# Kernel optimization log

Hardware: AMD Instinct MI355X
Metric: run time of the kernel (lower is better)

## Reference

```python
import jax, jax.numpy as jnp
import numpy as np

B = 1
H_IMG, W_IMG = 64, 64
NF = H_IMG * W_IMG          # 4096 front/query tokens
NS = 1024                   # satellite tokens (32x32 grid)
SAT_IN, FRONT_IN = 768, 320
NH, HD = 8, 64
MD = NH * HD                # 512
GHID, GHD = 128, 16
GMD = NH * GHD              # 128
GEO_RATIO, ROPE_BASE = 0.5, 10000.0
LAMBDA_GEO, LAMBDA_GEOM = 1.0, 1.0
EPS = 1e-5


def _linear(x, w, b):
    return x @ w.T + b


def _layernorm(x, g, b):
    m = x.mean(-1, keepdims=True)
    v = jnp.var(x, axis=-1, keepdims=True)
    return (x - m) / jnp.sqrt(v + EPS) * g + b


def _georope(t, xy):
    """Continuous 2D (x,y) rotary embedding on the first GEO_RATIO fraction of head_dim.
    t: [B,NH,N,HD], xy: [B,N,2]."""
    rot = int(HD * GEO_RATIO)       # rotated dims (32)
    axis = rot // 2                 # dims per spatial axis (16)
    half = axis // 2                # frequency pairs per axis (8)
    inv_freq = ROPE_BASE ** (-jnp.arange(half, dtype=t.dtype) / half)

    def rot_axis(a, coord):
        th = coord[:, None, :, None] * inv_freq   # [B,1,N,half]
        c, s = jnp.cos(th), jnp.sin(th)
        a1, a2 = a[..., :half], a[..., half:]
        return jnp.concatenate([a1 * c - a2 * s, a1 * s + a2 * c], axis=-1)

    tx = rot_axis(t[..., :axis], xy[..., 0])
    ty = rot_axis(t[..., axis:rot], xy[..., 1])
    return jnp.concatenate([tx, ty, t[..., rot:]], axis=-1)


def _heads(x, hd):
    b, n, _ = x.shape
    return x.reshape(b, n, NH, hd).transpose(0, 2, 1, 3)


def setup_inputs() -> dict:
    key = jax.random.key(0)
    ks = iter(jax.random.split(key, 64))

    def w(*shape):
        return jax.random.normal(next(ks), shape, jnp.float32) / np.sqrt(shape[-1]).astype(np.float32)

    z = lambda n: jnp.zeros((n,), jnp.float32)
    o = lambda n: jnp.ones((n,), jnp.float32)
    return {
        "front_feat": jax.random.normal(next(ks), (B, FRONT_IN, H_IMG, W_IMG), jnp.float32),
        "front_bev_xy": jax.random.uniform(next(ks), (B, NF, 2), jnp.float32, -1.0, 1.0),
        "sat_tokens": jax.random.normal(next(ks), (B, NS, SAT_IN), jnp.float32),
        "sat_xy": jax.random.uniform(next(ks), (B, NS, 2), jnp.float32, -1.0, 1.0),
        "front_plucker": jax.random.normal(next(ks), (B, NF, 6), jnp.float32),
        "pos_w1": w(MD, 2), "pos_b1": z(MD), "pos_w2": w(MD, MD), "pos_b2": z(MD),
        "fa_w": w(MD, FRONT_IN), "fa_b": z(MD), "fa_ln_g": o(MD), "fa_ln_b": z(MD),
        "qn_g": o(MD), "qn_b": z(MD),
        "sa_w": w(MD, SAT_IN), "sa_b": z(MD), "sa_ln_g": o(MD), "sa_ln_b": z(MD),
        "wq": w(MD, MD), "bq": z(MD), "wk": w(MD, MD), "bk": z(MD), "wv": w(MD, MD), "bv": z(MD),
        "plk_w1": w(GHID, 6), "plk_b1": z(GHID), "plk_w2": w(GHID, GHID), "plk_b2": z(GHID),
        "sxy_w1": w(GHID, 2), "sxy_b1": z(GHID), "sxy_w2": w(GHID, GHID), "sxy_b2": z(GHID),
        "gqn_g": o(GHID), "gqn_b": z(GHID), "gkn_g": o(GHID), "gkn_b": z(GHID),
        "wqg": w(GMD, GHID), "bqg": z(GMD), "wkg": w(GMD, GHID), "bkg": z(GMD),
    }


def reference(front_feat, front_bev_xy, sat_tokens, sat_xy, front_plucker,
              pos_w1, pos_b1, pos_w2, pos_b2, fa_w, fa_b, fa_ln_g, fa_ln_b,
              qn_g, qn_b, sa_w, sa_b, sa_ln_g, sa_ln_b, wq, bq, wk, bk, wv, bv,
              plk_w1, plk_b1, plk_w2, plk_b2, sxy_w1, sxy_b1, sxy_w2, sxy_b2,
              gqn_g, gqn_b, gkn_g, gkn_b, wqg, bqg, wkg, bkg):
    b = front_feat.shape[0]
    ff = front_feat.reshape(b, FRONT_IN, NF).transpose(0, 2, 1)      # [B,NF,C]
    pos = _linear(jax.nn.silu(_linear(front_bev_xy, pos_w1, pos_b1)), pos_w2, pos_b2)
    feat = _layernorm(_linear(ff, fa_w, fa_b), fa_ln_g, fa_ln_b)
    q_embed = _layernorm(pos + feat, qn_g, qn_b)
    sat_feat = _layernorm(_linear(sat_tokens, sa_w, sa_b), sa_ln_g, sa_ln_b)
    q = _heads(_linear(q_embed, wq, bq), HD)                         # [B,H,NF,HD]
    k = _heads(_linear(sat_feat, wk, bk), HD)                        # [B,H,NS,HD]
    v = _heads(_linear(sat_feat, wv, bv), HD)
    qr = _georope(q, front_bev_xy)
    kr = _georope(k, sat_xy)
    logits = jnp.einsum('bhqd,bhkd->bhqk', qr, kr) / np.float32(np.sqrt(HD))
    # learned geometric Q/K stream (Plucker rays vs sat xy)
    plk = _layernorm(_linear(jax.nn.silu(_linear(front_plucker, plk_w1, plk_b1)), plk_w2, plk_b2), gqn_g, gqn_b)
    sgf = _layernorm(_linear(jax.nn.silu(_linear(sat_xy, sxy_w1, sxy_b1)), sxy_w2, sxy_b2), gkn_g, gkn_b)
    qg = _heads(_linear(plk, wqg, bqg), GHD)
    kg = _heads(_linear(sgf, wkg, bkg), GHD)
    logits = logits + LAMBDA_GEOM * (jnp.einsum('bhqd,bhkd->bhqk', qg, kg) / np.float32(np.sqrt(GHD)))
    # additive pairwise squared-distance bias, broadcast over heads
    dist2 = ((front_bev_xy[:, :, None, :] - sat_xy[:, None, :, :]) ** 2).sum(-1)   # [B,NF,NS]
    logits = logits - LAMBDA_GEO * dist2[:, None]
    attn = jax.nn.softmax(logits, axis=-1)
    read = jnp.einsum('bhqk,bhkd->bhqd', attn, v)
    return read.transpose(0, 2, 1, 3).reshape(b, NF, MD)
```

## Files before the change

### kernel.cpp

```cpp
#include <hip/hip_runtime.h>
#include <hip/hip_bf16.h>
#include <stdint.h>

#define NF 4096
#define NS 1024
#define MD 512
#define HD 64
#define DA 96
#define GHID 128

#define L2E 1.44269504f
#define S2L 1.6986436f
#define SMAX 12.0f
#define NSPLIT 2

typedef unsigned short u16;
typedef __attribute__((ext_vector_type(8))) short bf8v;
typedef __attribute__((ext_vector_type(4))) float f4v;

__device__ __forceinline__ u16 f2bf(float f) {
  __hip_bfloat16 h = __float2bfloat16(f);
  return __builtin_bit_cast(u16, h);
}
__device__ __forceinline__ float bf2f(u16 u) {
  union { unsigned u; float f; } v; v.u = ((unsigned)u) << 16; return v.f;
}
__device__ __forceinline__ f4v mfma16(bf8v a, bf8v b, f4v c) {
  return __builtin_amdgcn_mfma_f32_16x16x32_bf16(a, b, c, 0, 0, 0);
}
__device__ __forceinline__ void gld16(const void* g, void* l) {
  __builtin_amdgcn_global_load_lds(
      (const __attribute__((address_space(1))) unsigned int*)g,
      (__attribute__((address_space(3))) unsigned int*)l, 16, 0, 0);
}

__device__ __forceinline__ size_t kfidx(int h, int n, int d) {
  return ((((size_t)(h * 16 + (n >> 6)) * 4 + ((n >> 4) & 3)) * 3 + (d >> 5)) * 64
          + ((d >> 3) & 3) * 16 + (n & 15)) * 8 + (d & 7);
}
__device__ __forceinline__ size_t vfidx(int h, int n, int dv) {
  return ((((size_t)(h * 16 + (n >> 6)) * 2 + ((n >> 5) & 1)) * 4 + (dv >> 4)) * 64
          + ((n >> 3) & 3) * 16 + (dv & 15)) * 8 + (n & 7);
}

#define OFF_POSW2 0
#define OFF_FAW   262144
#define OFF_SAW   425984
#define OFF_WQ    819200
#define OFF_WKV   1081344
#define OFF_PLKW2 1605632
#define OFF_SXYW2 1622016
#define OFF_WQG   1638400
#define OFF_WKG   1654784
#define OFF_SATT  1671168
#define TOTW      2457600

#define EPI_OUT   0
#define EPI_ROPE  1
#define EPI_VT    2
#define EPI_GEO   3
#define EPI_ROPEK 4
#define EPI_GEOK  5

__global__ __launch_bounds__(256) void k_l0(
    const float* __restrict__ s0, const float* __restrict__ s1,
    const float* __restrict__ s2, const float* __restrict__ s3,
    const float* __restrict__ s4, const float* __restrict__ s5,
    const float* __restrict__ s6, const float* __restrict__ s7,
    const float* __restrict__ s8, const float* __restrict__ s9,
    const float* __restrict__ s10, u16* __restrict__ pool,
    const float* __restrict__ bk, const float* __restrict__ bv,
    float* __restrict__ bkv,
    const float* __restrict__ ff, u16* __restrict__ ffT,
    const float* __restrict__ in0, const float* __restrict__ w0,
    const float* __restrict__ b0, u16* __restrict__ o0,
    const float* __restrict__ in1, const float* __restrict__ w1,
    const float* __restrict__ b1, u16* __restrict__ o1,
    const float* __restrict__ in2, const float* __restrict__ w2,
    const float* __restrict__ b2, u16* __restrict__ o2,
    u16* __restrict__ Qaug, u16* __restrict__ Kf, float* __restrict__ kk2) {
  __shared__ u16 sT[32][72];
  int blk = blockIdx.x, t = threadIdx.x;
  if (blk < 2401) {
    int i4 = blk * 256 + t;
    if (i4 < TOTW / 4) {
      int idx = i4 * 4;
      const float* src; int off;
      if      (idx < OFF_FAW)   { src = s0;  off = OFF_POSW2; }
      else if (idx < OFF_SAW)   { src = s1;  off = OFF_FAW; }
      else if (idx < OFF_WQ)    { src = s2;  off = OFF_SAW; }
      else if (idx < OFF_WKV)   { src = s3;  off = OFF_WQ; }
      else if (idx < 1343488)   { src = s4;  off = OFF_WKV; }
      else if (idx < OFF_PLKW2) { src = s5;  off = 1343488; }
      else if (idx < OFF_SXYW2) { src = s6;  off = OFF_PLKW2; }
      else if (idx < OFF_WQG)   { src = s7;  off = OFF_SXYW2; }
      else if (idx < OFF_WKG)   { src = s8;  off = OFF_WQG; }
      else if (idx < OFF_SATT)  { src = s9;  off = OFF_WKG; }
      else                      { src = s10; off = OFF_SATT; }
      float4 v = *(const float4*)(src + (idx - off));
      ushort4 o;
      o.x = f2bf(v.x); o.y = f2bf(v.y); o.z = f2bf(v.z); o.w = f2bf(v.w);
      *(ushort4*)(pool + idx) = o;
    } else if (i4 < TOTW / 4 + 256) {
      int j = (i4 - TOTW / 4) * 4;
#pragma unroll
      for (int e = 0; e < 4; ++e) {
        int b = j + e;
        bkv[b] = (b < 512) ? bk[b] : bv[b - 512];
      }
    }
  } else if (blk < 3041) {
    int lb = blk - 2401;
    int n0 = (lb & 63) * 64, c0 = (lb >> 6) * 32;
    {
      int cr = t >> 3, nc = (t & 7) * 8;
      const float* src = ff + (size_t)(c0 + cr) * NF + n0 + nc;
      float4 v0 = *(const float4*)src, v1 = *(const float4*)(src + 4);
      bf8v p;
      p[0]=(short)f2bf(v0.x); p[1]=(short)f2bf(v0.y); p[2]=(short)f2bf(v0.z); p[3]=(short)f2bf(v0.w);
      p[4]=(short)f2bf(v1.x); p[5]=(short)f2bf(v1.y); p[6]=(short)f2bf(v1.z); p[7]=(short)f2bf(v1.w);
      *(bf8v*)&sT[cr][nc] = p;
    }
    __syncthreads();
    {
      int r = t >> 2, cc = (t & 3) * 8;
      bf8v p;
#pragma unroll
      for (int e = 0; e < 8; ++e) p[e] = (short)sT[cc + e][r];
      *(bf8v*)(ffT + (size_t)(n0 + r) * 320 + c0 + cc) = p;
    }
  } else if (blk < 13793) {
    int lb = blk - 3041;
    const float *in, *w, *b; u16* o; int mlog, K, idx;
    if (lb < 8192)       { in = in0; w = w0; b = b0; o = o0; mlog = 9; K = 2; idx = lb * 256 + t; }
    else if (lb < 10240) { in = in1; w = w1; b = b1; o = o1; mlog = 7; K = 6; idx = (lb - 8192) * 256 + t; }
    else                 { in = in2; w = w2; b = b2; o = o2; mlog = 7; K = 2; idx = (lb - 10240) * 256 + t; }
    int M = 1 << mlog;
    int n = idx >> mlog, m = idx & (M - 1);
    float acc = b[m];
    for (int k = 0; k < K; ++k) acc += in[n * K + k] * w[m * K + k];
    o[idx] = f2bf(acc / (1.f + __expf(-acc)));
  } else {
    int id = (blk - 13793) * 256 + t;
    int side = id >= NF * 8;
    int lid = side ? id - NF * 8 : id;
    int n = lid >> 3, h = lid & 7;
    const float* xy = side ? in2 : in0;
    float x = xy[n * 2], y = xy[n * 2 + 1];
    bf8v p0, z;
#pragma unroll
    for (int e = 0; e < 8; ++e) { p0[e] = 0; z[e] = 0; }
    p0[0] = (short)f2bf(S2L * x);
    p0[1] = (short)f2bf(S2L * y);
    if (!side) {
      u16* dst = Qaug + ((size_t)h * NF + n) * DA + 80;
      *(bf8v*)dst = p0;
      *(bf8v*)(dst + 8) = z;
    } else {
      int t8 = n >> 6, jj = (n >> 4) & 3, l16 = n & 15;
      size_t base = (((size_t)(h * 16 + t8) * 4 + jj) * 3 + 2) * 64;
      *(bf8v*)(Kf + (base + 32 + l16) * 8) = p0;
      *(bf8v*)(Kf + (base + 48 + l16) * 8) = z;
      if (h == 0) kk2[n] = L2E * (x * x + y * y) + SMAX;
    }
  }
}

__device__ __forceinline__ void gemm_body128(const u16* __restrict__ A, const u16* __restrict__ W,
                                             const float* __restrict__ bias, u16* __restrict__ out,
                                             int m0, int n0, int N, int K) {
  __shared__ u16 sA[2][128 * 64];
  __shared__ u16 sB[2][64 * 64];
  const int tid = threadIdx.x, w = tid >> 6, lane = tid & 63;
  const int l16 = lane & 15, lh = lane >> 4;

  f4v acc[2][4];
#pragma unroll
  for (int m = 0; m < 2; ++m)
#pragma unroll
    for (int j = 0; j < 4; ++j) acc[m][j] = (f4v){0.f, 0.f, 0.f, 0.f};

  auto stageA = [&](int buf, int k0) {
#pragma unroll
    for (int i = 0; i < 4; ++i) {
      int c = i * 256 + tid;
      int row = c >> 3, cp = c & 7;
      int sc_ = cp ^ (row & 7);
      gld16(A + (size_t)(m0 + row) * K + k0 + sc_ * 8, &sA[buf][c * 8]);
    }
  };
  auto stageB = [&](int buf, int k0) {
#pragma unroll
    for (int i = 0; i < 2; ++i) {
      int c = i * 256 + tid;
      int row = c >> 3, cp = c & 7;
      int sc_ = cp ^ (row & 7);
      gld16(W + (size_t)(n0 + row) * K + k0 + sc_ * 8, &sB[buf][c * 8]);
    }
  };

  stageA(0, 0); stageB(0, 0);
  __syncthreads();
  const int NK = K >> 6;
  for (int ks = 0; ks < NK; ++ks) {
    int nb = ks & 1;
    if (ks + 1 < NK) { stageA(nb ^ 1, (ks + 1) * 64); stageB(nb ^ 1, (ks + 1) * 64); }
#pragma unroll
    for (int kk = 0; kk < 2; ++kk) {
      bf8v af[2], bfr[4];
#pragma unroll
      for (int m = 0; m < 2; ++m) {
        int row = w * 32 + m * 16 + l16;
        int cp = (kk * 4 + lh) ^ (row & 7);
        af[m] = *(const bf8v*)&sA[nb][row * 64 + cp * 8];
      }
#pragma unroll
      for (int j = 0; j < 4; ++j) {
        int row = j * 16 + l16;
        int cp = (kk * 4 + lh) ^ (row & 7);
        bfr[j] = *(const bf8v*)&sB[nb][row * 64 + cp * 8];
      }
#pragma unroll
      for (int m = 0; m < 2; ++m)
#pragma unroll
        for (int j = 0; j < 4; ++j) acc[m][j] = mfma16(af[m], bfr[j], acc[m][j]);
    }
    __syncthreads();
  }
#pragma unroll
  for (int m = 0; m < 2; ++m) {
    int grow = m0 + w * 32 + m * 16 + (lh << 2);
#pragma unroll
    for (int j = 0; j < 4; ++j) {
      int gcol = n0 + j * 16 + l16;
      float bvs = bias ? bias[gcol] : 0.f;
#pragma unroll
      for (int r = 0; r < 4; ++r)
        out[(size_t)(grow + r) * N + gcol] = f2bf(acc[m][j][r] + bvs);
    }
  }
}

__device__ __forceinline__ void gemm_body(const u16* __restrict__ A, const u16* __restrict__ W,
                                          const float* __restrict__ bias, u16* __restrict__ out,
                                          int m0, int n0, int N, int K,
                                          int mode, float scale, const float* __restrict__ xy,
                                          u16* __restrict__ aug, int nrows) {
  constexpr int MR = 2, NR = 2;
  __shared__ u16 sA[2][64 * 64];
  __shared__ u16 sB[2][64 * 64];
  const int tid = threadIdx.x, w = tid >> 6, lane = tid & 63;
  const int l16 = lane & 15, lh = lane >> 4;
  const int wr = w >> 1, wc = w & 1;

  f4v acc[MR][NR];
#pragma unroll
  for (int m = 0; m < MR; ++m)
#pragma unroll
    for (int j = 0; j < NR; ++j) acc[m][j] = (f4v){0.f, 0.f, 0.f, 0.f};

  auto stageA = [&](int buf, int k0) {
#pragma unroll
    for (int i = 0; i < 2; ++i) {
      int c = i * 256 + tid;
      int row = c >> 3, cp = c & 7;
      int sc_ = cp ^ (row & 7);
      gld16(A + (size_t)(m0 + row) * K + k0 + sc_ * 8, &sA[buf][c * 8]);
    }
  };
  auto stageB = [&](int buf, int k0) {
#pragma unroll
    for (int i = 0; i < 2; ++i) {
      int c = i * 256 + tid;
      int row = c >> 3, cp = c & 7;
      int sc_ = cp ^ (row & 7);
      gld16(W + (size_t)(n0 + row) * K + k0 + sc_ * 8, &sB[buf][c * 8]);
    }
  };

  stageA(0, 0); stageB(0, 0);
  __syncthreads();
  const int NK = K >> 6;
  for (int ks = 0; ks < NK; ++ks) {
    int nb = ks & 1;
    if (ks + 1 < NK) { stageA(nb ^ 1, (ks + 1) * 64); stageB(nb ^ 1, (ks + 1) * 64); }
#pragma unroll
    for (int kk = 0; kk < 2; ++kk) {
      bf8v af[MR], bfr[NR];
#pragma unroll
      for (int m = 0; m < MR; ++m) {
        int row = wr * 32 + m * 16 + l16;
        int cp = (kk * 4 + lh) ^ (row & 7);
        af[m] = *(const bf8v*)&sA[nb][row * 64 + cp * 8];
      }
#pragma unroll
      for (int j = 0; j < NR; ++j) {
        int row = wc * 32 + j * 16 + l16;
        int cp = (kk * 4 + lh) ^ (row & 7);
        bfr[j] = *(const bf8v*)&sB[nb][row * 64 + cp * 8];
      }
#pragma unroll
      for (int m = 0; m < MR; ++m)
#pragma unroll
        for (int j = 0; j < NR; ++j) acc[m][j] = mfma16(af[m], bfr[j], acc[m][j]);
    }
    __syncthreads();
  }

  if (mode == EPI_OUT) {
#pragma unroll
    for (int m = 0; m < MR; ++m) {
      int grow = m0 + wr * 32 + m * 16 + (lh << 2);
#pragma unroll
      for (int j = 0; j < NR; ++j) {
        int gcol = n0 + wc * 32 + j * 16 + l16;
        float bvs = bias ? bias[gcol] : 0.f;
#pragma unroll
        for (int r = 0; r < 4; ++r)
          out[(size_t)(grow + r) * N + gcol] = f2bf(acc[m][j][r] + bvs);
      }
    }
  } else if (mode == EPI_ROPE || mode == EPI_ROPEK) {
    float fr = __expf(-(float)(l16 & 7) * 1.1512925465f);
#pragma unroll
    for (int m = 0; m < MR; ++m) {
      int grow = m0 + wr * 32 + m * 16 + (lh << 2);
#pragma unroll
      for (int j = 0; j < NR; ++j) {
        int gcol = n0 + wc * 32 + j * 16 + l16;
        int h = gcol >> 6, d = gcol & 63;
        float bvs = bias[gcol];
#pragma unroll
        for (int r = 0; r < 4; ++r) {
          int n = grow + r;
          float val = acc[m][j][r] + bvs;
          float part = __shfl_xor(val, 8);
          float outv = val;
          if (wc == 0) {
            float2 c2 = ((const float2*)xy)[n];
            float coord = j ? c2.y : c2.x;
            float sn, cs;
            __sincosf(coord * fr, &sn, &cs);
            outv = (l16 & 8) ? (part * sn + val * cs) : (val * cs - part * sn);
          }
          if (mode == EPI_ROPE)
            aug[((size_t)h * nrows + n) * DA + d] = f2bf(outv * scale);
          else
            aug[kfidx(h, n, d)] = f2bf(outv * scale);
        }
      }
    }
  } else if (mode == EPI_VT) {
#pragma unroll
    for (int m = 0; m < MR; ++m) {
      int grow = m0 + wr * 32 + m * 16 + (lh << 2);
#pragma unroll
      for (int j = 0; j < NR; ++j) {
        int gcol = n0 + wc * 32 + j * 16 + l16;
        int vcol = gcol - 512;
        int h = vcol >> 6, dv = vcol & 63;
        float bvs = bias[gcol];
        ushort4 o;
        o.x = f2bf(acc[m][j][0] + bvs);
        o.y = f2bf(acc[m][j][1] + bvs);
        o.z = f2bf(acc[m][j][2] + bvs);
        o.w = f2bf(acc[m][j][3] + bvs);
        *(ushort4*)(aug + vfidx(h, grow, dv)) = o;
      }
    }
  } else {
#pragma unroll
    for (int m = 0; m < MR; ++m) {
      int grow = m0 + wr * 32 + m * 16 + (lh << 2);
#pragma unroll
      for (int j = 0; j < NR; ++j) {
        int gcol = n0 + wc * 32 + j * 16 + l16;
        int h = gcol >> 4, dg = gcol & 15;
        float bvs = bias[gcol];
#pragma unroll
        for (int r = 0; r < 4; ++r) {
          float ov = (acc[m][j][r] + bvs) * scale;
          if (mode == EPI_GEO)
            aug[((size_t)h * nrows + grow + r) * DA + 64 + dg] = f2bf(ov);
          else
            aug[kfidx(h, grow + r, 64 + dg)] = f2bf(ov);
        }
      }
    }
  }
}

struct GP { const u16* A; const u16* W; const float* bias; u16* out;
            int K; int N; int M; int mode; float scale; const float* xy;
            u16* aug; int nrows; };

__device__ __forceinline__ void gemm_dispatch128(const GP& g, int blk) {
  int mt = g.M >> 7;
  int m0 = (blk % mt) * 128, n0 = (blk / mt) * 64;
  gemm_body128(g.A, g.W, g.bias, g.out, m0, n0, g.N, g.K);
}
__device__ __forceinline__ void gemm_dispatch(const GP& g, int blk) {
  int mt = g.M >> 6;
  int m0 = (blk % mt) * 64, n0 = (blk / mt) * 64;
  gemm_body(g.A, g.W, g.bias, g.out, m0, n0, g.N, g.K,
            g.mode, g.scale, g.xy, g.aug, g.nrows);
}

__global__ __launch_bounds__(256) void k_gemm_L1(GP a, GP b, GP c, GP d, GP e) {
  int blk = blockIdx.x;
  if (blk < 256)       gemm_dispatch128(a, blk);
  else if (blk < 512)  gemm_dispatch128(b, blk - 256);
  else if (blk < 576)  gemm_dispatch128(c, blk - 512);
  else if (blk < 640)  gemm_dispatch128(d, blk - 576);
  else                 gemm_dispatch128(e, blk - 640);
}
__global__ __launch_bounds__(256) void k_gemm_L2(GP a, GP b, GP c, GP d, u16* Vfp) {
  int blk = blockIdx.x;
  if (blk < 512) {
    gemm_dispatch(a, blk);
  } else if (blk < 768) {
    int lb = blk - 512;
    int m0 = (lb & 15) * 64, n0 = (lb >> 4) * 64;
    if (n0 >= 512)
      gemm_body(b.A, b.W, b.bias, b.out, m0, n0, b.N, b.K, EPI_VT, 1.f, nullptr, Vfp, NS);
    else
      gemm_body(b.A, b.W, b.bias, b.out, m0, n0, b.N, b.K, b.mode, b.scale, b.xy, b.aug, b.nrows);
  } else if (blk < 896) {
    gemm_dispatch(c, blk - 768);
  } else {
    gemm_dispatch(d, blk - 896);
  }
}

__global__ __launch_bounds__(256) void k_ln_all(
    const u16* __restrict__ feat_pre, const u16* __restrict__ pos,
    const float* __restrict__ fg, const float* __restrict__ fb,
    const float* __restrict__ qg, const float* __restrict__ qb2,
    u16* __restrict__ q_embed,
    const u16* __restrict__ satf_pre, const float* __restrict__ sg,
    const float* __restrict__ sb, u16* __restrict__ satf,
    const u16* __restrict__ ginq, const u16* __restrict__ gink,
    const float* __restrict__ ggq, const float* __restrict__ gbq,
    const float* __restrict__ ggk, const float* __restrict__ gbk,
    u16* __restrict__ goutq, u16* __restrict__ goutk) {
  int blk = blockIdx.x;
  int w = threadIdx.x >> 6, lane = threadIdx.x & 63;
  if (blk < 1024) {
    int row = blk * 4 + w;
    bf8v v = *(const bf8v*)(feat_pre + (size_t)row * 512 + lane * 8);
    float x[8];
#pragma unroll
    for (int e = 0; e < 8; ++e) x[e] = bf2f((u16)v[e]);
    float s = 0.f, q = 0.f;
#pragma unroll
    for (int e = 0; e < 8; ++e) { s += x[e]; q += x[e] * x[e]; }
#pragma unroll
    for (int mm = 1; mm < 64; mm <<= 1) { s += __shfl_xor(s, mm); q += __shfl_xor(q, mm); }
    float mean = s / 512.f, var = q / 512.f - mean * mean;
    float rstd = rsqrtf(var + 1e-5f);
    bf8v vp = *(const bf8v*)(pos + (size_t)row * 512 + lane * 8);
#pragma unroll
    for (int e = 0; e < 8; ++e)
      x[e] = (x[e] - mean) * rstd * fg[lane * 8 + e] + fb[lane * 8 + e] + bf2f((u16)vp[e]);
    s = 0.f; q = 0.f;
#pragma unroll
    for (int e = 0; e < 8; ++e) { s += x[e]; q += x[e] * x[e]; }
#pragma unroll
    for (int mm = 1; mm < 64; mm <<= 1) { s += __shfl_xor(s, mm); q += __shfl_xor(q, mm); }
    mean = s / 512.f; var = q / 512.f - mean * mean;
    rstd = rsqrtf(var + 1e-5f);
    bf8v ov;
#pragma unroll
    for (int e = 0; e < 8; ++e)
      ov[e] = (short)f2bf((x[e] - mean) * rstd * qg[lane * 8 + e] + qb2[lane * 8 + e]);
    *(bf8v*)(q_embed + (size_t)row * 512 + lane * 8) = ov;
  } else if (blk < 1280) {
    int row = (blk - 1024) * 4 + w;
    bf8v v = *(const bf8v*)(satf_pre + (size_t)row * 512 + lane * 8);
    float x[8];
#pragma unroll
    for (int e = 0; e < 8; ++e) x[e] = bf2f((u16)v[e]);
    float s = 0.f, q = 0.f;
#pragma unroll
    for (int e = 0; e < 8; ++e) { s += x[e]; q += x[e] * x[e]; }
#pragma unroll
    for (int mm = 1; mm < 64; mm <<= 1) { s += __shfl_xor(s, mm); q += __shfl_xor(q, mm); }
    float mean = s / 512.f, var = q / 512.f - mean * mean;
    float rstd = rsqrtf(var + 1e-5f);
    bf8v ov;
#pragma unroll
    for (int e = 0; e < 8; ++e)
      ov[e] = (short)f2bf((x[e] - mean) * rstd * sg[lane * 8 + e] + sb[lane * 8 + e]);
    *(bf8v*)(satf + (size_t)row * 512 + lane * 8) = ov;
  } else {
    int row = (blk - 1280) * 4 + w;
    const u16* in; const float *g, *b; u16* out;
    if (row < 4096) { in = ginq; g = ggq; b = gbq; out = goutq; }
    else { row -= 4096; in = gink; g = ggk; b = gbk; out = goutk; }
    uint32_t v = *(const uint32_t*)(in + (size_t)row * 128 + lane * 2);
    float x0 = bf2f((u16)(v & 0xffff)), x1 = bf2f((u16)(v >> 16));
    float s = x0 + x1, q = x0 * x0 + x1 * x1;
#pragma unroll
    for (int mm = 1; mm < 64; mm <<= 1) { s += __shfl_xor(s, mm); q += __shfl_xor(q, mm); }
    float mean = s / 128.f, var = q / 128.f - mean * mean;
    float rstd = rsqrtf(var + 1e-5f);
    u16 o0 = f2bf((x0 - mean) * rstd * g[lane * 2] + b[lane * 2]);
    u16 o1 = f2bf((x1 - mean) * rstd * g[lane * 2 + 1] + b[lane * 2 + 1]);
    *(uint32_t*)(out + (size_t)row * 128 + lane * 2) = (uint32_t)o0 | ((uint32_t)o1 << 16);
  }
}

__global__ __launch_bounds__(256, 4) void k_flash(const u16* __restrict__ Qa,
                                                  const u16* __restrict__ Kf,
                                                  const u16* __restrict__ Vf,
                                                  const float* __restrict__ kk2,
                                                  u16* __restrict__ Opart,
                                                  float* __restrict__ lbuf) {
  const int h = blockIdx.y, qb = blockIdx.x, sp = blockIdx.z;
  const int tid = threadIdx.x, w = tid >> 6, lane = tid & 63;
  const int l16 = lane & 15, lh = lane >> 4;
  __shared__ u16 sP[4][16][68];
  __shared__ float sKK[512];

  ((float2*)sKK)[tid] = ((const float2*)(kk2 + sp * 512))[tid];

  const int qrow = qb * 64 + w * 16 + l16;
  bf8v qf[3];
#pragma unroll
  for (int c = 0; c < 3; ++c)
    qf[c] = *(const bf8v*)(Qa + (size_t)(h * NF + qrow) * DA + c * 32 + lh * 8);

  bf8v ONES;
#pragma unroll
  for (int i = 0; i < 8; ++i) ONES[i] = (short)0x3F80;

  const int crow = qb * 64 + w * 16 + (lh << 2);
  float l_run[4] = {0.f, 0.f, 0.f, 0.f};
  f4v accO[4];
#pragma unroll
  for (int d = 0; d < 4; ++d) accO[d] = (f4v){0.f, 0.f, 0.f, 0.f};

  const int kt0 = sp * (NS / 64 / NSPLIT);
  __syncthreads();

  const int NT = NS / 64 / NSPLIT;
  for (int t8 = 0; t8 < NT; ++t8) {
    const int T = kt0 + t8;
    const u16* kfb = Kf + (size_t)(h * 16 + T) * 4 * 3 * 64 * 8;
    const u16* vfb = Vf + (size_t)(h * 16 + T) * 2 * 4 * 64 * 8;
#pragma unroll
    for (int j = 0; j < 4; ++j) {
      f4v s4 = (f4v){0.f, 0.f, 0.f, 0.f};
#pragma unroll
      for (int c = 0; c < 3; ++c) {
        bf8v kf = *(const bf8v*)(kfb + (size_t)((j * 3 + c) * 64 + lane) * 8);
        s4 = mfma16(qf[c], kf, s4);
      }
      float ck = sKK[t8 * 64 + j * 16 + l16];
#pragma unroll
      for (int r = 0; r < 4; ++r) {
        float pv = exp2f(s4[r] - ck);
        sP[w][(lh << 2) + r][j * 16 + l16] = f2bf(pv);
      }
    }
    bf8v pf0 = *(const bf8v*)&sP[w][l16][lh * 8];
    bf8v pf1 = *(const bf8v*)&sP[w][l16][32 + lh * 8];
    f4v ls = (f4v){0.f, 0.f, 0.f, 0.f};
    ls = mfma16(pf0, ONES, ls);
    ls = mfma16(pf1, ONES, ls);
#pragma unroll
    for (int r = 0; r < 4; ++r) l_run[r] += ls[r];
#pragma unroll
    for (int c = 0; c < 2; ++c) {
      bf8v pf = (c == 0) ? pf0 : pf1;
#pragma unroll
      for (int d = 0; d < 4; ++d) {
        bf8v vf = *(const bf8v*)(vfb + (size_t)((c * 4 + d) * 64 + lane) * 8);
        accO[d] = mfma16(pf, vf, accO[d]);
      }
    }
  }
  size_t obase = (size_t)(sp * 8 + h) * NF + crow;
#pragma unroll
  for (int d = 0; d < 4; ++d)
#pragma unroll
    for (int r = 0; r < 4; ++r)
      Opart[(obase + r) * 64 + d * 16 + l16] = f2bf(accO[d][r]);
  if (l16 == 0) {
#pragma unroll
    for (int r = 0; r < 4; ++r) lbuf[obase + r] = l_run[r];
  }
}

__global__ void k_combine(const u16* __restrict__ Opart, const float* __restrict__ lbuf,
                          float* __restrict__ out) {
  int i4 = blockIdx.x * 256 + threadIdx.x;
  int n = i4 >> 7;
  int c4 = i4 & 127, h = c4 >> 4, d4 = c4 & 15;
  float l = 0.f, ox = 0.f, oy = 0.f, oz = 0.f, ow = 0.f;
#pragma unroll
  for (int s2 = 0; s2 < NSPLIT; ++s2) {
    size_t base = (size_t)(s2 * 8 + h) * NF + n;
    l += lbuf[base];
    ushort4 a = ((const ushort4*)(Opart + base * 64))[d4];
    ox += bf2f(a.x); oy += bf2f(a.y); oz += bf2f(a.z); ow += bf2f(a.w);
  }
  float rl = 1.f / l;
  ((float4*)out)[i4] = make_float4(ox * rl, oy * rl, oz * rl, ow * rl);
}

extern "C" void kernel_launch(void* const* d_in, const int* in_sizes, int n_in,
                              void* d_out, int out_size, void* d_ws, size_t ws_size,
                              hipStream_t stream) {
  (void)in_sizes; (void)n_in; (void)out_size; (void)ws_size;
  const float* front_feat = (const float*)d_in[0];
  const float* bev_xy     = (const float*)d_in[1];
  const float* sat_tokens = (const float*)d_in[2];
  const float* sat_xy     = (const float*)d_in[3];
  const float* plucker    = (const float*)d_in[4];
  const float* pos_w1 = (const float*)d_in[5];
  const float* pos_b1 = (const float*)d_in[6];
  const float* pos_w2 = (const float*)d_in[7];
  const float* pos_b2 = (const float*)d_in[8];
  const float* fa_w   = (const float*)d_in[9];
  const float* fa_b   = (const float*)d_in[10];
  const float* fa_ln_g = (const float*)d_in[11];
  const float* fa_ln_b = (const float*)d_in[12];
  const float* qn_g   = (const float*)d_in[13];
  const float* qn_b   = (const float*)d_in[14];
  const float* sa_w   = (const float*)d_in[15];
  const float* sa_b   = (const float*)d_in[16];
  const float* sa_ln_g = (const float*)d_in[17];
  const float* sa_ln_b = (const float*)d_in[18];
  const float* wq = (const float*)d_in[19];
  const float* bq = (const float*)d_in[20];
  const float* wk = (const float*)d_in[21];
  const float* bk = (const float*)d_in[22];
  const float* wv = (const float*)d_in[23];
  const float* bv = (const float*)d_in[24];
  const float* plk_w1 = (const float*)d_in[25];
  const float* plk_b1 = (const float*)d_in[26];
  const float* plk_w2 = (const float*)d_in[27];
  const float* plk_b2 = (const float*)d_in[28];
  const float* sxy_w1 = (const float*)d_in[29];
  const float* sxy_b1 = (const float*)d_in[30];
  const float* sxy_w2 = (const float*)d_in[31];
  const float* sxy_b2 = (const float*)d_in[32];
  const float* gqn_g = (const float*)d_in[33];
  const float* gqn_b = (const float*)d_in[34];
  const float* gkn_g = (const float*)d_in[35];
  const float* gkn_b = (const float*)d_in[36];
  const float* wqg = (const float*)d_in[37];
  const float* bqg = (const float*)d_in[38];
  const float* wkg = (const float*)d_in[39];
  const float* bkg = (const float*)d_in[40];

  char* ws = (char*)d_ws;
  size_t off = 0;
  auto alloc = [&](size_t bytes) {
    size_t r = off;
    off += (bytes + 255) & ~(size_t)255;
    return r;
  };
  u16*   wpool   = (u16*)(ws + alloc((size_t)TOTW * 2));
  float* bkv     = (float*)(ws + alloc(1024 * 4));
  u16*   ffT     = (u16*)(ws + alloc((size_t)NF * 320 * 2));
  u16*   pos_h   = (u16*)(ws + alloc((size_t)NF * MD * 2));
  u16*   plk_h   = (u16*)(ws + alloc((size_t)NF * GHID * 2));
  u16*   sxy_h   = (u16*)(ws + alloc((size_t)NS * GHID * 2));
  u16*   pos     = (u16*)(ws + alloc((size_t)NF * MD * 2));
  u16*   feat_pre= (u16*)(ws + alloc((size_t)NF * MD * 2));
  u16*   satf_pre= (u16*)(ws + alloc((size_t)NS * MD * 2));
  u16*   satf    = (u16*)(ws + alloc((size_t)NS * MD * 2));
  u16*   q_embed = (u16*)(ws + alloc((size_t)NF * MD * 2));
  u16*   plk2    = (u16*)(ws + alloc((size_t)NF * GHID * 2));
  u16*   sxy2    = (u16*)(ws + alloc((size_t)NS * GHID * 2));
  u16*   Qaug    = (u16*)(ws + alloc((size_t)8 * NF * DA * 2));
  u16*   Kf      = (u16*)(ws + alloc((size_t)8 * NS * DA * 2));
  u16*   Vf      = (u16*)(ws + alloc((size_t)8 * HD * NS * 2));
  float* kk2     = (float*)(ws + alloc((size_t)NS * 4));
  u16*   Opart   = (u16*)(ws + alloc((size_t)NSPLIT * 8 * NF * 64 * 2));
  float* lbuf    = (float*)(ws + alloc((size_t)NSPLIT * 8 * NF * 4));
  u16* plk_ln = plk_h;
  u16* sgf    = sxy_h;

  dim3 b256(256);
  k_l0<<<dim3(13953), b256, 0, stream>>>(
      pos_w2, fa_w, sa_w, wq, wk, wv, plk_w2, sxy_w2, wqg, wkg, sat_tokens,
      wpool, bk, bv, bkv, front_feat, ffT,
      bev_xy, pos_w1, pos_b1, pos_h,
      plucker, plk_w1, plk_b1, plk_h,
      sat_xy, sxy_w1, sxy_b1, sxy_h,
      Qaug, Kf, kk2);

  GP gpos {pos_h, wpool + OFF_POSW2, pos_b2, pos, 512, 512, 4096, EPI_OUT, 0.f, nullptr, nullptr, 0};
  GP gfeat{ffT, wpool + OFF_FAW, fa_b, feat_pre, 320, 512, 4096, EPI_OUT, 0.f, nullptr, nullptr, 0};
  GP gsat {wpool + OFF_SATT, wpool + OFF_SAW, sa_b, satf_pre, 768, 512, 1024, EPI_OUT, 0.f, nullptr, nullptr, 0};
  GP ggq1 {plk_h, wpool + OFF_PLKW2, plk_b2, plk2, 128, 128, 4096, EPI_OUT, 0.f, nullptr, nullptr, 0};
  GP ggk1 {sxy_h, wpool + OFF_SXYW2, sxy_b2, sxy2, 128, 128, 1024, EPI_OUT, 0.f, nullptr, nullptr, 0};
  k_gemm_L1<<<dim3(656), b256, 0, stream>>>(gpos, gfeat, gsat, ggq1, ggk1);

  k_ln_all<<<dim3(2560), b256, 0, stream>>>(
      feat_pre, pos, fa_ln_g, fa_ln_b, qn_g, qn_b, q_embed,
      satf_pre, sa_ln_g, sa_ln_b, satf,
      plk2, sxy2, gqn_g, gqn_b, gkn_g, gkn_b, plk_ln, sgf);

  GP gq  {q_embed, wpool + OFF_WQ, bq, nullptr, 512, 512, 4096, EPI_ROPE, 0.125f * L2E, bev_xy, Qaug, NF};
  GP gkv {satf, wpool + OFF_WKV, bkv, nullptr, 512, 1024, 1024, EPI_ROPEK, 1.f, sat_xy, Kf, NS};
  GP ggq2{plk_ln, wpool + OFF_WQG, bqg, nullptr, 128, 128, 4096, EPI_GEO, 0.25f * L2E, nullptr, Qaug, NF};
  GP ggk2{sgf, wpool + OFF_WKG, bkg, nullptr, 128, 128, 1024, EPI_GEOK, 1.f, nullptr, Kf, NS};
  k_gemm_L2<<<dim3(928), b256, 0, stream>>>(gq, gkv, ggq2, ggk2, Vf);

  k_flash<<<dim3(NF / 64, 8, NSPLIT), b256, 0, stream>>>(Qaug, Kf, Vf, kk2, Opart, lbuf);
  k_combine<<<dim3(NF * MD / 4 / 256), b256, 0, stream>>>(Opart, lbuf, (float*)d_out);
}
```

Measured before the change: 79.74 us.

## Merge split-K flash halves within one block and drop combine kernel

```diff
diff --git a/kernel.cpp b/kernel.cpp
--- a/kernel.cpp
+++ b/kernel.cpp
@@ -12,7 +12,6 @@
 #define L2E 1.44269504f
 #define S2L 1.6986436f
 #define SMAX 12.0f
-#define NSPLIT 2
 
 typedef unsigned short u16;
 typedef __attribute__((ext_vector_type(8))) short bf8v;
@@ -510,19 +509,22 @@
   }
 }
 
-__global__ __launch_bounds__(256, 4) void k_flash(const u16* __restrict__ Qa,
+__global__ __launch_bounds__(512, 2) void k_flash(const u16* __restrict__ Qa,
                                                   const u16* __restrict__ Kf,
                                                   const u16* __restrict__ Vf,
                                                   const float* __restrict__ kk2,
-                                                  u16* __restrict__ Opart,
-                                                  float* __restrict__ lbuf) {
-  const int h = blockIdx.y, qb = blockIdx.x, sp = blockIdx.z;
-  const int tid = threadIdx.x, w = tid >> 6, lane = tid & 63;
+                                                  float* __restrict__ out) {
+  const int h = blockIdx.y, qb = blockIdx.x;
+  const int tid = threadIdx.x;
+  const int half = tid >> 8, t = tid & 255;
+  const int w = t >> 6, lane = t & 63;
   const int l16 = lane & 15, lh = lane >> 4;
-  __shared__ u16 sP[4][16][68];
-  __shared__ float sKK[512];
-
-  ((float2*)sKK)[tid] = ((const float2*)(kk2 + sp * 512))[tid];
+  __shared__ u16 sP[8][16][68];
+  __shared__ float sKK[1024];
+  __shared__ float xO[256 * 16];
+  __shared__ float xl[256 * 4];
+
+  ((float2*)sKK)[tid] = ((const float2*)kk2)[tid];
 
   const int qrow = qb * 64 + w * 16 + l16;
   bf8v qf[3];
@@ -540,12 +542,10 @@
 #pragma unroll
   for (int d = 0; d < 4; ++d) accO[d] = (f4v){0.f, 0.f, 0.f, 0.f};
 
-  const int kt0 = sp * (NS / 64 / NSPLIT);
   __syncthreads();
 
-  const int NT = NS / 64 / NSPLIT;
-  for (int t8 = 0; t8 < NT; ++t8) {
-    const int T = kt0 + t8;
+  for (int t8 = 0; t8 < 8; ++t8) {
+    const int T = half * 8 + t8;
     const u16* kfb = Kf + (size_t)(h * 16 + T) * 4 * 3 * 64 * 8;
     const u16* vfb = Vf + (size_t)(h * 16 + T) * 2 * 4 * 64 * 8;
 #pragma unroll
@@ -556,15 +556,15 @@
         bf8v kf = *(const bf8v*)(kfb + (size_t)((j * 3 + c) * 64 + lane) * 8);
         s4 = mfma16(qf[c], kf, s4);
       }
-      float ck = sKK[t8 * 64 + j * 16 + l16];
+      float ck = sKK[T * 64 + j * 16 + l16];
 #pragma unroll
       for (int r = 0; r < 4; ++r) {
         float pv = exp2f(s4[r] - ck);
-        sP[w][(lh << 2) + r][j * 16 + l16] = f2bf(pv);
-      }
-    }
-    bf8v pf0 = *(const bf8v*)&sP[w][l16][lh * 8];
-    bf8v pf1 = *(const bf8v*)&sP[w][l16][32 + lh * 8];
+        sP[half * 4 + w][(lh << 2) + r][j * 16 + l16] = f2bf(pv);
+      }
+    }
+    bf8v pf0 = *(const bf8v*)&sP[half * 4 + w][l16][lh * 8];
+    bf8v pf1 = *(const bf8v*)&sP[half * 4 + w][l16][32 + lh * 8];
     f4v ls = (f4v){0.f, 0.f, 0.f, 0.f};
     ls = mfma16(pf0, ONES, ls);
     ls = mfma16(pf1, ONES, ls);
@@ -580,33 +580,28 @@
       }
     }
   }
-  size_t obase = (size_t)(sp * 8 + h) * NF + crow;
-#pragma unroll
-  for (int d = 0; d < 4; ++d)
-#pragma unroll
-    for (int r = 0; r < 4; ++r)
-      Opart[(obase + r) * 64 + d * 16 + l16] = f2bf(accO[d][r]);
-  if (l16 == 0) {
-#pragma unroll
-    for (int r = 0; r < 4; ++r) lbuf[obase + r] = l_run[r];
-  }
-}
-
-__global__ void k_combine(const u16* __restrict__ Opart, const float* __restrict__ lbuf,
-                          float* __restrict__ out) {
-  int i4 = blockIdx.x * 256 + threadIdx.x;
-  int n = i4 >> 7;
-  int c4 = i4 & 127, h = c4 >> 4, d4 = c4 & 15;
-  float l = 0.f, ox = 0.f, oy = 0.f, oz = 0.f, ow = 0.f;
-#pragma unroll
-  for (int s2 = 0; s2 < NSPLIT; ++s2) {
-    size_t base = (size_t)(s2 * 8 + h) * NF + n;
-    l += lbuf[base];
-    ushort4 a = ((const ushort4*)(Opart + base * 64))[d4];
-    ox += bf2f(a.x); oy += bf2f(a.y); oz += bf2f(a.z); ow += bf2f(a.w);
-  }
-  float rl = 1.f / l;
-  ((float4*)out)[i4] = make_float4(ox * rl, oy * rl, oz * rl, ow * rl);
+
+  if (half == 1) {
+#pragma unroll
+    for (int d = 0; d < 4; ++d)
+#pragma unroll
+      for (int r = 0; r < 4; ++r) xO[t * 16 + d * 4 + r] = accO[d][r];
+#pragma unroll
+    for (int r = 0; r < 4; ++r) xl[t * 4 + r] = l_run[r];
+  }
+  __syncthreads();
+  if (half == 0) {
+    float rl[4];
+#pragma unroll
+    for (int r = 0; r < 4; ++r) rl[r] = 1.f / (l_run[r] + xl[t * 4 + r]);
+#pragma unroll
+    for (int d = 0; d < 4; ++d)
+#pragma unroll
+      for (int r = 0; r < 4; ++r) {
+        float o = (accO[d][r] + xO[t * 16 + d * 4 + r]) * rl[r];
+        out[(size_t)(crow + r) * MD + h * 64 + d * 16 + l16] = o;
+      }
+  }
 }
 
 extern "C" void kernel_launch(void* const* d_in, const int* in_sizes, int n_in,
@@ -679,8 +674,6 @@
   u16*   Kf      = (u16*)(ws + alloc((size_t)8 * NS * DA * 2));
   u16*   Vf      = (u16*)(ws + alloc((size_t)8 * HD * NS * 2));
   float* kk2     = (float*)(ws + alloc((size_t)NS * 4));
-  u16*   Opart   = (u16*)(ws + alloc((size_t)NSPLIT * 8 * NF * 64 * 2));
-  float* lbuf    = (float*)(ws + alloc((size_t)NSPLIT * 8 * NF * 4));
   u16* plk_ln = plk_h;
   u16* sgf    = sxy_h;
 
@@ -711,6 +704,5 @@
   GP ggk2{sgf, wpool + OFF_WKG, bkg, nullptr, 128, 128, 1024, EPI_GEOK, 1.f, nullptr, Kf, NS};
   k_gemm_L2<<<dim3(928), b256, 0, stream>>>(gq, gkv, ggq2, ggk2, Vf);
 
-  k_flash<<<dim3(NF / 64, 8, NSPLIT), b256, 0, stream>>>(Qaug, Kf, Vf, kk2, Opart, lbuf);
-  k_combine<<<dim3(NF * MD / 4 / 256), b256, 0, stream>>>(Opart, lbuf, (float*)d_out);
-}
+  k_flash<<<dim3(NF / 64, 8), dim3(512), 0, stream>>>(Qaug, Kf, Vf, kk2, (float*)d_out);
+}
```

New measurement: 83.05 us. 1.04x slower.
